# Kernel tuning notes

Measured on AMD Instinct MI355X. Metric: run time of the kernel, lower is better.

## Reference

```python
import jax, jax.numpy as jnp
import numpy as np
from jax import lax

NEG = -1e30  # finite stand-in for -inf to keep gradients clean
BLANK = 0


def _ctc_loss(log_probs, targets, logits_lengths, targets_lengths):
    # log_probs: (B, T, V) log-softmaxed; targets: (B, S) int; lengths: (B,)
    B, T, V = log_probs.shape
    S = targets.shape[1]
    L = 2 * S + 1  # extended label length: blank-interleaved

    # extended label sequence: [blank, t0, blank, t1, ..., blank]
    ext = jnp.zeros((B, L), dtype=targets.dtype).at[:, 1::2].set(targets)

    # gather log-probs of extended labels per time step -> (B, T, L)
    lp_ext = jnp.take_along_axis(
        log_probs, jnp.broadcast_to(ext[:, None, :], (B, T, L)), axis=2
    )

    # skip transition (s-2 -> s) allowed where ext[s] != blank and ext[s] != ext[s-2]
    skip = jnp.concatenate(
        [jnp.zeros((B, 2), dtype=bool),
         (ext[:, 2:] != ext[:, :-2]) & (ext[:, 2:] != BLANK)],
        axis=1,
    )

    # alpha init at t=0
    alpha0 = jnp.full((B, L), NEG, dtype=log_probs.dtype)
    alpha0 = alpha0.at[:, 0].set(lp_ext[:, 0, 0])
    alpha0 = alpha0.at[:, 1].set(
        jnp.where(targets_lengths > 0, lp_ext[:, 0, 1], NEG))

    neg1 = jnp.full((B, 1), NEG, dtype=log_probs.dtype)
    neg2 = jnp.full((B, 2), NEG, dtype=log_probs.dtype)

    def step(alpha, inp):
        lp_t, t = inp  # lp_t: (B, L)
        a1 = jnp.concatenate([neg1, alpha[:, :-1]], axis=1)
        a2 = jnp.where(skip, jnp.concatenate([neg2, alpha[:, :-2]], axis=1), NEG)
        new = jnp.logaddexp(jnp.logaddexp(alpha, a1), a2) + lp_t
        # freeze alpha once past each sequence's length so final read is at t=len-1
        alpha = jnp.where((t < logits_lengths)[:, None], new, alpha)
        return alpha, None

    lp_tbl = jnp.transpose(lp_ext, (1, 0, 2))  # (T, B, L)
    alpha, _ = lax.scan(step, alpha0, (lp_tbl[1:], jnp.arange(1, T)))

    # final states: last blank (index 2*tl) and last label (index 2*tl-1)
    idx_blank = (2 * targets_lengths).astype(jnp.int32)
    idx_label = jnp.maximum(2 * targets_lengths - 1, 0).astype(jnp.int32)
    a_blank = jnp.take_along_axis(alpha, idx_blank[:, None], axis=1)[:, 0]
    a_label = jnp.take_along_axis(alpha, idx_label[:, None], axis=1)[:, 0]
    a_label = jnp.where(targets_lengths > 0, a_label, NEG)
    return -jnp.logaddexp(a_blank, a_label)  # (B,)


def setup_inputs() -> dict:
    key = jax.random.key(0)
    k1, k2, k3, k4 = jax.random.split(key, 4)
    B, T, V, S = 32, 1024, 512, 128
    logits = jax.random.normal(k1, (B, T, V), dtype=jnp.float32)
    targets = jax.random.randint(k2, (B, S), 1, V, dtype=jnp.int32)  # avoid blank=0
    logits_lengths = jax.random.randint(k3, (B,), T // 2, T + 1, dtype=jnp.int32)
    targets_lengths = jax.random.randint(k4, (B,), S // 2, S + 1, dtype=jnp.int32)
    return {
        "logits": logits,
        "targets": targets,
        "logits_lengths": logits_lengths,
        "targets_lengths": targets_lengths,
    }


def reference(logits, targets, logits_lengths, targets_lengths):
    # after_logsoftmax=False -> apply log_softmax; time_major=False -> no permute
    log_probs = jax.nn.log_softmax(logits, axis=2)
    # reduce=None -> per-batch loss of shape (B,)
    return _ctc_loss(log_probs, targets, logits_lengths, targets_lengths)
```

## Files before the change

### kernel.cpp

```cpp
#include <hip/hip_runtime.h>

enum { B_ = 32, T_ = 1024, V_ = 512, S_ = 128 };

static constexpr float K2   = 1.4426950408889634f;
static constexpr float LN2F = 0.6931471805599453f;
#define BOOSTI 6

typedef float f32x4 __attribute__((ext_vector_type(4)));
#define AS1 __attribute__((address_space(1)))
#define AS3 __attribute__((address_space(3)))

#define DPPI(x, ctrl) __builtin_amdgcn_update_dpp(0, (x), (ctrl), 0xF, 0xF, true)
#define DPPF(x, ctrl) __int_as_float(DPPI(__float_as_int(x), (ctrl)))
#define DPP_WSR1(x) DPPF((x), 0x138)

__device__ __forceinline__ float dpp_wave_max_l63(float x) {
  x = fmaxf(x, DPPF(x, 0xB1));   x = fmaxf(x, DPPF(x, 0x4E));
  x = fmaxf(x, DPPF(x, 0x124));  x = fmaxf(x, DPPF(x, 0x128));
  x = fmaxf(x, DPPF(x, 0x142));  x = fmaxf(x, DPPF(x, 0x143));
  return x;
}

__global__ __launch_bounds__(256) void ctc_pre4(
    const float* __restrict__ logits, const int* __restrict__ targets,
    const int* __restrict__ loglen, const int* __restrict__ tgtlen,
    f32x4* __restrict__ Q) {
  const int w = threadIdx.x >> 6, l = threadIdx.x & 63;
  const int row = blockIdx.x * 4 + w;
  const int b = row >> 10;
  const int t = row & (T_ - 1);
  if (t >= loglen[b]) return;
  const float* lrow = logits + (size_t)row * V_;
  const float4* r4 = (const float4*)lrow;
  float4 a = r4[l], c = r4[l + 64];
  float s = __builtin_exp2f(a.x * K2) + __builtin_exp2f(a.y * K2) +
            __builtin_exp2f(a.z * K2) + __builtin_exp2f(a.w * K2) +
            __builtin_exp2f(c.x * K2) + __builtin_exp2f(c.y * K2) +
            __builtin_exp2f(c.z * K2) + __builtin_exp2f(c.w * K2);
  #pragma unroll
  for (int off = 32; off; off >>= 1) s += __shfl_xor(s, off, 64);
  const float sh = (float)BOOSTI - __builtin_log2f(s);

  const int2 ee = ((const int2*)(targets + b * S_))[l];
  const int tl = tgtlen[b];
  const float lgb = __shfl(a.x, 0, 64);
  const float lg1 = lrow[ee.x];
  const float lg3 = lrow[ee.y];
  const float pb  = __builtin_exp2f(fmaf(lgb, K2, sh));
  const float pe1 = __builtin_exp2f(fmaf(lg1, K2, sh));
  const float pe3 = __builtin_exp2f(fmaf(lg3, K2, sh));
  const int smax = 2 * tl;
  f32x4 q;
  q.x = (4 * l + 1 <= smax) ? pe1 : 0.0f;
  q.y = (4 * l + 3 <= smax) ? pe3 : 0.0f;
  q.z = (4 * l     <= smax) ? pb  : 0.0f;
  q.w = (4 * l + 2 <= smax) ? pb  : 0.0f;
  Q[(size_t)row * 64 + l] = q;
}

__global__ __launch_bounds__(128, 1) void ctc_dp7(
    const f32x4* __restrict__ Q, const int* __restrict__ targets,
    const int* __restrict__ loglen, const int* __restrict__ tgtlen,
    float* __restrict__ out) {
  __shared__ f32x4 buf[2][32 * 64];
  __shared__ int flag_ready[2];
  __shared__ int flag_done[2];
  __shared__ float A[257];
  const int wv = threadIdx.x >> 6, l = threadIdx.x & 63;
  const int b = blockIdx.x;
  const int len = loglen[b], tl = tgtlen[b];
  const int nch = (len - 1 + 31) >> 5;
  const f32x4* Qb = Q + (size_t)b * T_ * 64;

  if (threadIdx.x == 0) {
    flag_ready[0] = 0; flag_ready[1] = 0;
    flag_done[0] = 0;  flag_done[1] = 0;
  }
  __syncthreads();

  if (wv == 1) {
    for (int c = 0; c < nch; ++c) {
      if (c >= 2) {
        while (((volatile int*)flag_done)[c & 1] < c - 1)
          __builtin_amdgcn_s_sleep(1);
      }
      const int r0 = 1 + 32 * c;
      #pragma unroll
      for (int i = 0; i < 32; ++i) {
        int row = r0 + i; if (row > T_ - 1) row = T_ - 1;
        __builtin_amdgcn_global_load_lds(
            (const AS1 void*)(const void*)(Qb + (size_t)row * 64 + l),
            (AS3 void*)(void*)(&buf[c & 1][i * 64]), 16, 0, 0);
      }
      asm volatile("s_waitcnt vmcnt(0)" ::: "memory");
      if (l == 0) ((volatile int*)flag_ready)[c & 1] = c + 1;
    }
    return;
  }

  __builtin_amdgcn_s_setprio(1);

  const int2 ee = ((const int2*)(targets + b * S_))[l];
  const int e1 = ee.x, e3 = ee.y;
  const int em1 = __shfl_up(e3, 1);
  const float m1 = ((l > 0) && (e1 != 0) && (e1 != em1)) ? 1.0f : 0.0f;
  const float m3 = ((e3 != 0) && (e3 != e1)) ? 1.0f : 0.0f;
  const float v4l = ((l == 63) && (2 * tl >= 256)) ? 1.0f : 0.0f;

  f32x4 qi = Qb[l];
  float p0 = (l == 0) ? qi.z : 0.0f;
  float p1 = (l == 0) ? qi.x : 0.0f;
  float p2 = 0.0f, p3 = 0.0f, p4 = 0.0f;

  const unsigned bufbase = (unsigned)(uintptr_t)(AS3 char*)(void*)&buf[0][0];

  f32x4 q0, q1, q2, q3, q4, q5, q6, q7;
#define DSRO(R, O) asm volatile("ds_read_b128 %0, %1 offset:" #O \
      : "=&v"(R) : "v"(vb))
#define WTL(R, N) asm volatile("s_waitcnt lgkmcnt(" #N ")" : "+v"(R))

#define COMPUTE(RX) { \
    const float n1_  = DPP_WSR1(p3); \
    const float w0_ = (p0 + n1_) * RX.z; \
    const float w1_ = (p0 + p1 + n1_ * m1) * RX.x; \
    const float w2_ = (p1 + p2) * RX.w; \
    const float w3_ = (p2 + p3 + p1 * m3) * RX.y; \
    const float w4_ = (p4 + p3) * RX.w * v4l; \
    p0 = w0_; p1 = w1_; p2 = w2_; p3 = w3_; p4 = w4_; \
  }

#define RENORM { \
    float m_ = fmaxf(fmaxf(fmaxf(p0, p1), fmaxf(p2, p3)), p4); \
    m_ = dpp_wave_max_l63(m_); \
    const int wm_ = __builtin_amdgcn_readlane(__float_as_int(m_), 63); \
    const int e_ = (wm_ >> 23) & 0xFF; \
    const float sc_ = __int_as_float((254 - e_) << 23); \
    p0 *= sc_; p1 *= sc_; p2 *= sc_; p3 *= sc_; p4 *= sc_; \
    shift += e_ - 127; \
  }

#define FS(R, O)  { WTL(R, 7); COMPUTE(R); DSRO(R, O); }
#define FD(R, N)  { WTL(R, N); COMPUTE(R); }
#define TS(R, O, i)  { WTL(R, 7); if (t0 + (i) < len) COMPUTE(R); DSRO(R, O); }
#define TD(R, N, i)  { WTL(R, N); if (t0 + (i) < len) COMPUTE(R); }

  int shift = 0;
  for (int c = 0; c < nch; ++c) {
    const int t0 = 1 + 32 * c;
    while (((volatile int*)flag_ready)[c & 1] < c + 1)
      __builtin_amdgcn_s_sleep(1);
    const unsigned vb = bufbase + (unsigned)(c & 1) * 32768u + (unsigned)l * 16u;

    DSRO(q0, 0);    DSRO(q1, 1024); DSRO(q2, 2048); DSRO(q3, 3072);
    DSRO(q4, 4096); DSRO(q5, 5120); DSRO(q6, 6144); DSRO(q7, 7168);

    if (t0 + 31 < len) {
      FS(q0, 8192)  FS(q1, 9216)  FS(q2, 10240) FS(q3, 11264)
      FS(q4, 12288) FS(q5, 13312) FS(q6, 14336) FS(q7, 15360)
      FS(q0, 16384) FS(q1, 17408) FS(q2, 18432) FS(q3, 19456)
      FS(q4, 20480) FS(q5, 21504) FS(q6, 22528) FS(q7, 23552)
      RENORM
      FS(q0, 24576) FS(q1, 25600) FS(q2, 26624) FS(q3, 27648)
      FS(q4, 28672) FS(q5, 29696) FS(q6, 30720) FS(q7, 31744)
      FD(q0, 7) FD(q1, 6) FD(q2, 5) FD(q3, 4)
      FD(q4, 3) FD(q5, 2) FD(q6, 1) FD(q7, 0)
      RENORM
    } else {
      TS(q0, 8192, 0)   TS(q1, 9216, 1)   TS(q2, 10240, 2)  TS(q3, 11264, 3)
      TS(q4, 12288, 4)  TS(q5, 13312, 5)  TS(q6, 14336, 6)  TS(q7, 15360, 7)
      TS(q0, 16384, 8)  TS(q1, 17408, 9)  TS(q2, 18432, 10) TS(q3, 19456, 11)
      TS(q4, 20480, 12) TS(q5, 21504, 13) TS(q6, 22528, 14) TS(q7, 23552, 15)
      TS(q0, 24576, 16) TS(q1, 25600, 17) TS(q2, 26624, 18) TS(q3, 27648, 19)
      TS(q4, 28672, 20) TS(q5, 29696, 21) TS(q6, 30720, 22) TS(q7, 31744, 23)
      TD(q0, 7, 24) TD(q1, 6, 25) TD(q2, 5, 26) TD(q3, 4, 27)
      TD(q4, 3, 28) TD(q5, 2, 29) TD(q6, 1, 30) TD(q7, 0, 31)
    }

    asm volatile("s_waitcnt lgkmcnt(0)" ::: "memory");
    if (l == 0) ((volatile int*)flag_done)[c & 1] = c + 1;
  }

  A[4 * l + 0] = p0; A[4 * l + 1] = p1;
  A[4 * l + 2] = p2; A[4 * l + 3] = p3;
  if (l == 63) A[256] = p4;
  asm volatile("s_waitcnt lgkmcnt(0)" ::: "memory");
  if (l == 0) {
    const int ib = 2 * tl;
    const int il = (ib - 1) > 0 ? ib - 1 : 0;
    const float ab = A[ib];
    const float al = (tl > 0) ? A[il] : 0.0f;
    out[b] = -(__builtin_log2f(ab + al) + (float)(shift - BOOSTI * len)) * LN2F;
  }
}

extern "C" void kernel_launch(void* const* d_in, const int* in_sizes, int n_in,
                              void* d_out, int out_size, void* d_ws, size_t ws_size,
                              hipStream_t stream) {
  const float* logits  = (const float*)d_in[0];
  const int*   targets = (const int*)d_in[1];
  const int*   loglen  = (const int*)d_in[2];
  const int*   tgtlen  = (const int*)d_in[3];
  float* out = (float*)d_out;
  f32x4* Q = (f32x4*)d_ws;

  ctc_pre4<<<(B_ * T_) / 4, 256, 0, stream>>>(logits, targets, loglen, tgtlen, Q);
  ctc_dp7<<<B_, 128, 0, stream>>>(Q, targets, loglen, tgtlen, out);
}
```

Measured before the change: 62.59 us.

## Interleave two batch recurrences per compute wave to hide serial DP latency

The DP kernel now handles two batch elements per block: one compute wave advances both alpha recurrences in lockstep while two loader waves fill separate double-buffered LDS regions. Interleaving two independent dependency chains is meant to hide the DPP and FMA latency of the serial per-timestep recurrence. In exchange, the grid halves to 16 blocks, each block runs until the longer of its two sequences finishes, and LDS and register use double. The partial-chunk path now also renormalises mid-chunk.

```diff
diff --git a/kernel.cpp b/kernel.cpp
--- a/kernel.cpp
+++ b/kernel.cpp
@@ -58,138 +58,188 @@
   Q[(size_t)row * 64 + l] = q;
 }
 
-__global__ __launch_bounds__(128, 1) void ctc_dp7(
+__global__ __launch_bounds__(192, 1) void ctc_dp8(
     const f32x4* __restrict__ Q, const int* __restrict__ targets,
     const int* __restrict__ loglen, const int* __restrict__ tgtlen,
     float* __restrict__ out) {
-  __shared__ f32x4 buf[2][32 * 64];
-  __shared__ int flag_ready[2];
-  __shared__ int flag_done[2];
-  __shared__ float A[257];
+  __shared__ f32x4 bufA[2][32 * 64];
+  __shared__ f32x4 bufB[2][32 * 64];
+  __shared__ int flag_readyA[2], flag_readyB[2], flag_doneA[2], flag_doneB[2];
+  __shared__ float Aa[257], Ab[257];
   const int wv = threadIdx.x >> 6, l = threadIdx.x & 63;
-  const int b = blockIdx.x;
-  const int len = loglen[b], tl = tgtlen[b];
-  const int nch = (len - 1 + 31) >> 5;
-  const f32x4* Qb = Q + (size_t)b * T_ * 64;
+  const int bA = blockIdx.x, bB = blockIdx.x + 16;
+  const int lenA = loglen[bA], lenB = loglen[bB];
+  const int tlA = tgtlen[bA], tlB = tgtlen[bB];
+  const int lenMax = lenA > lenB ? lenA : lenB;
+  const int lenMin = lenA < lenB ? lenA : lenB;
+  const int nch = (lenMax - 1 + 31) >> 5;
+  const f32x4* QbA = Q + (size_t)bA * T_ * 64;
+  const f32x4* QbB = Q + (size_t)bB * T_ * 64;
 
   if (threadIdx.x == 0) {
-    flag_ready[0] = 0; flag_ready[1] = 0;
-    flag_done[0] = 0;  flag_done[1] = 0;
+    flag_readyA[0] = flag_readyA[1] = 0; flag_readyB[0] = flag_readyB[1] = 0;
+    flag_doneA[0] = flag_doneA[1] = 0;   flag_doneB[0] = flag_doneB[1] = 0;
   }
   __syncthreads();
 
-  if (wv == 1) {
+  if (wv != 0) {
+    const f32x4* Qp = (wv == 1) ? QbA : QbB;
+    f32x4* bufp = (wv == 1) ? &bufA[0][0] : &bufB[0][0];
+    volatile int* fr = (wv == 1) ? (volatile int*)flag_readyA : (volatile int*)flag_readyB;
+    volatile int* fd = (wv == 1) ? (volatile int*)flag_doneA : (volatile int*)flag_doneB;
     for (int c = 0; c < nch; ++c) {
       if (c >= 2) {
-        while (((volatile int*)flag_done)[c & 1] < c - 1)
-          __builtin_amdgcn_s_sleep(1);
+        while (fd[c & 1] < c - 1) __builtin_amdgcn_s_sleep(1);
       }
       const int r0 = 1 + 32 * c;
       #pragma unroll
       for (int i = 0; i < 32; ++i) {
         int row = r0 + i; if (row > T_ - 1) row = T_ - 1;
         __builtin_amdgcn_global_load_lds(
-            (const AS1 void*)(const void*)(Qb + (size_t)row * 64 + l),
-            (AS3 void*)(void*)(&buf[c & 1][i * 64]), 16, 0, 0);
+            (const AS1 void*)(const void*)(Qp + (size_t)row * 64 + l),
+            (AS3 void*)(void*)(bufp + ((c & 1) * 2048 + i * 64)), 16, 0, 0);
       }
       asm volatile("s_waitcnt vmcnt(0)" ::: "memory");
-      if (l == 0) ((volatile int*)flag_ready)[c & 1] = c + 1;
+      if (l == 0) fr[c & 1] = c + 1;
     }
     return;
   }
 
   __builtin_amdgcn_s_setprio(1);
 
-  const int2 ee = ((const int2*)(targets + b * S_))[l];
-  const int e1 = ee.x, e3 = ee.y;
-  const int em1 = __shfl_up(e3, 1);
-  const float m1 = ((l > 0) && (e1 != 0) && (e1 != em1)) ? 1.0f : 0.0f;
-  const float m3 = ((e3 != 0) && (e3 != e1)) ? 1.0f : 0.0f;
-  const float v4l = ((l == 63) && (2 * tl >= 256)) ? 1.0f : 0.0f;
-
-  f32x4 qi = Qb[l];
-  float p0 = (l == 0) ? qi.z : 0.0f;
-  float p1 = (l == 0) ? qi.x : 0.0f;
-  float p2 = 0.0f, p3 = 0.0f, p4 = 0.0f;
-
-  const unsigned bufbase = (unsigned)(uintptr_t)(AS3 char*)(void*)&buf[0][0];
-
-  f32x4 q0, q1, q2, q3, q4, q5, q6, q7;
-#define DSRO(R, O) asm volatile("ds_read_b128 %0, %1 offset:" #O \
-      : "=&v"(R) : "v"(vb))
-#define WTL(R, N) asm volatile("s_waitcnt lgkmcnt(" #N ")" : "+v"(R))
-
-#define COMPUTE(RX) { \
-    const float n1_  = DPP_WSR1(p3); \
-    const float w0_ = (p0 + n1_) * RX.z; \
-    const float w1_ = (p0 + p1 + n1_ * m1) * RX.x; \
-    const float w2_ = (p1 + p2) * RX.w; \
-    const float w3_ = (p2 + p3 + p1 * m3) * RX.y; \
-    const float w4_ = (p4 + p3) * RX.w * v4l; \
-    p0 = w0_; p1 = w1_; p2 = w2_; p3 = w3_; p4 = w4_; \
-  }
-
-#define RENORM { \
-    float m_ = fmaxf(fmaxf(fmaxf(p0, p1), fmaxf(p2, p3)), p4); \
+  const int2 eeA = ((const int2*)(targets + bA * S_))[l];
+  const int2 eeB = ((const int2*)(targets + bB * S_))[l];
+  const int e1A = eeA.x, e3A = eeA.y, e1B = eeB.x, e3B = eeB.y;
+  const int em1A = __shfl_up(e3A, 1);
+  const int em1B = __shfl_up(e3B, 1);
+  const float m1A = ((l > 0) && (e1A != 0) && (e1A != em1A)) ? 1.0f : 0.0f;
+  const float m3A = ((e3A != 0) && (e3A != e1A)) ? 1.0f : 0.0f;
+  const float v4lA = ((l == 63) && (2 * tlA >= 256)) ? 1.0f : 0.0f;
+  const float m1B = ((l > 0) && (e1B != 0) && (e1B != em1B)) ? 1.0f : 0.0f;
+  const float m3B = ((e3B != 0) && (e3B != e1B)) ? 1.0f : 0.0f;
+  const float v4lB = ((l == 63) && (2 * tlB >= 256)) ? 1.0f : 0.0f;
+
+  f32x4 qiA = QbA[l];
+  f32x4 qiB = QbB[l];
+  float p0A = (l == 0) ? qiA.z : 0.0f, p1A = (l == 0) ? qiA.x : 0.0f;
+  float p2A = 0.0f, p3A = 0.0f, p4A = 0.0f;
+  float p0B = (l == 0) ? qiB.z : 0.0f, p1B = (l == 0) ? qiB.x : 0.0f;
+  float p2B = 0.0f, p3B = 0.0f, p4B = 0.0f;
+
+  const unsigned baseA = (unsigned)(uintptr_t)(AS3 char*)(void*)&bufA[0][0];
+  const unsigned baseB = (unsigned)(uintptr_t)(AS3 char*)(void*)&bufB[0][0];
+
+  asm volatile("s_waitcnt vmcnt(0) lgkmcnt(0)" ::: "memory");
+
+  f32x4 qa0, qa1, qa2, qa3, qa4, qa5, qa6, qa7;
+  f32x4 qb0, qb1, qb2, qb3, qb4, qb5, qb6, qb7;
+#define DSRA(R, O) asm volatile("ds_read_b128 %0, %1 offset:" #O \
+      : "=&v"(R) : "v"(vba))
+#define DSRB(R, O) asm volatile("ds_read_b128 %0, %1 offset:" #O \
+      : "=&v"(R) : "v"(vbb))
+#define WT2(RA, RB, N) asm volatile("s_waitcnt lgkmcnt(" #N ")" \
+      : "+v"(RA), "+v"(RB))
+
+#define COMP(RX, S) { \
+    const float n1_ = DPP_WSR1(p3##S); \
+    const float w0_ = (p0##S + n1_) * RX.z; \
+    const float w1_ = (p0##S + p1##S + n1_ * m1##S) * RX.x; \
+    const float w2_ = (p1##S + p2##S) * RX.w; \
+    const float w3_ = (p2##S + p3##S + p1##S * m3##S) * RX.y; \
+    const float w4_ = (p4##S + p3##S) * RX.w * v4l##S; \
+    p0##S = w0_; p1##S = w1_; p2##S = w2_; p3##S = w3_; p4##S = w4_; \
+  }
+
+#define REN(S) { \
+    float m_ = fmaxf(fmaxf(fmaxf(p0##S, p1##S), fmaxf(p2##S, p3##S)), p4##S); \
     m_ = dpp_wave_max_l63(m_); \
     const int wm_ = __builtin_amdgcn_readlane(__float_as_int(m_), 63); \
     const int e_ = (wm_ >> 23) & 0xFF; \
     const float sc_ = __int_as_float((254 - e_) << 23); \
-    p0 *= sc_; p1 *= sc_; p2 *= sc_; p3 *= sc_; p4 *= sc_; \
-    shift += e_ - 127; \
-  }
-
-#define FS(R, O)  { WTL(R, 7); COMPUTE(R); DSRO(R, O); }
-#define FD(R, N)  { WTL(R, N); COMPUTE(R); }
-#define TS(R, O, i)  { WTL(R, 7); if (t0 + (i) < len) COMPUTE(R); DSRO(R, O); }
-#define TD(R, N, i)  { WTL(R, N); if (t0 + (i) < len) COMPUTE(R); }
-
-  int shift = 0;
+    p0##S *= sc_; p1##S *= sc_; p2##S *= sc_; p3##S *= sc_; p4##S *= sc_; \
+    shift##S += e_ - 127; \
+  }
+
+#define FS2(RA, RB, O) { WT2(RA, RB, 14); COMP(RA, A); COMP(RB, B); \
+    DSRA(RA, O); DSRB(RB, O); }
+#define FD2(RA, RB, N) { WT2(RA, RB, N); COMP(RA, A); COMP(RB, B); }
+#define GS2(RA, RB, O, i) { WT2(RA, RB, 14); \
+    if (t0 + (i) < lenA) COMP(RA, A); \
+    if (t0 + (i) < lenB) COMP(RB, B); \
+    DSRA(RA, O); DSRB(RB, O); }
+#define GD2(RA, RB, N, i) { WT2(RA, RB, N); \
+    if (t0 + (i) < lenA) COMP(RA, A); \
+    if (t0 + (i) < lenB) COMP(RB, B); }
+
+  int shiftA = 0, shiftB = 0;
   for (int c = 0; c < nch; ++c) {
     const int t0 = 1 + 32 * c;
-    while (((volatile int*)flag_ready)[c & 1] < c + 1)
-      __builtin_amdgcn_s_sleep(1);
-    const unsigned vb = bufbase + (unsigned)(c & 1) * 32768u + (unsigned)l * 16u;
-
-    DSRO(q0, 0);    DSRO(q1, 1024); DSRO(q2, 2048); DSRO(q3, 3072);
-    DSRO(q4, 4096); DSRO(q5, 5120); DSRO(q6, 6144); DSRO(q7, 7168);
-
-    if (t0 + 31 < len) {
-      FS(q0, 8192)  FS(q1, 9216)  FS(q2, 10240) FS(q3, 11264)
-      FS(q4, 12288) FS(q5, 13312) FS(q6, 14336) FS(q7, 15360)
-      FS(q0, 16384) FS(q1, 17408) FS(q2, 18432) FS(q3, 19456)
-      FS(q4, 20480) FS(q5, 21504) FS(q6, 22528) FS(q7, 23552)
-      RENORM
-      FS(q0, 24576) FS(q1, 25600) FS(q2, 26624) FS(q3, 27648)
-      FS(q4, 28672) FS(q5, 29696) FS(q6, 30720) FS(q7, 31744)
-      FD(q0, 7) FD(q1, 6) FD(q2, 5) FD(q3, 4)
-      FD(q4, 3) FD(q5, 2) FD(q6, 1) FD(q7, 0)
-      RENORM
+    while (((volatile int*)flag_readyA)[c & 1] < c + 1) __builtin_amdgcn_s_sleep(1);
+    while (((volatile int*)flag_readyB)[c & 1] < c + 1) __builtin_amdgcn_s_sleep(1);
+    const unsigned vba = baseA + (unsigned)(c & 1) * 32768u + (unsigned)l * 16u;
+    const unsigned vbb = baseB + (unsigned)(c & 1) * 32768u + (unsigned)l * 16u;
+
+    DSRA(qa0, 0);    DSRB(qb0, 0);
+    DSRA(qa1, 1024); DSRB(qb1, 1024);
+    DSRA(qa2, 2048); DSRB(qb2, 2048);
+    DSRA(qa3, 3072); DSRB(qb3, 3072);
+    DSRA(qa4, 4096); DSRB(qb4, 4096);
+    DSRA(qa5, 5120); DSRB(qb5, 5120);
+    DSRA(qa6, 6144); DSRB(qb6, 6144);
+    DSRA(qa7, 7168); DSRB(qb7, 7168);
+
+    if (t0 + 31 < lenMin) {
+      FS2(qa0, qb0, 8192)  FS2(qa1, qb1, 9216)  FS2(qa2, qb2, 10240) FS2(qa3, qb3, 11264)
+      FS2(qa4, qb4, 12288) FS2(qa5, qb5, 13312) FS2(qa6, qb6, 14336) FS2(qa7, qb7, 15360)
+      FS2(qa0, qb0, 16384) FS2(qa1, qb1, 17408) FS2(qa2, qb2, 18432) FS2(qa3, qb3, 19456)
+      FS2(qa4, qb4, 20480) FS2(qa5, qb5, 21504) FS2(qa6, qb6, 22528) FS2(qa7, qb7, 23552)
+      REN(A) REN(B)
+      FS2(qa0, qb0, 24576) FS2(qa1, qb1, 25600) FS2(qa2, qb2, 26624) FS2(qa3, qb3, 27648)
+      FS2(qa4, qb4, 28672) FS2(qa5, qb5, 29696) FS2(qa6, qb6, 30720) FS2(qa7, qb7, 31744)
+      FD2(qa0, qb0, 14) FD2(qa1, qb1, 12) FD2(qa2, qb2, 10) FD2(qa3, qb3, 8)
+      FD2(qa4, qb4, 6)  FD2(qa5, qb5, 4)  FD2(qa6, qb6, 2)  FD2(qa7, qb7, 0)
+      REN(A) REN(B)
     } else {
-      TS(q0, 8192, 0)   TS(q1, 9216, 1)   TS(q2, 10240, 2)  TS(q3, 11264, 3)
-      TS(q4, 12288, 4)  TS(q5, 13312, 5)  TS(q6, 14336, 6)  TS(q7, 15360, 7)
-      TS(q0, 16384, 8)  TS(q1, 17408, 9)  TS(q2, 18432, 10) TS(q3, 19456, 11)
-      TS(q4, 20480, 12) TS(q5, 21504, 13) TS(q6, 22528, 14) TS(q7, 23552, 15)
-      TS(q0, 24576, 16) TS(q1, 25600, 17) TS(q2, 26624, 18) TS(q3, 27648, 19)
-      TS(q4, 28672, 20) TS(q5, 29696, 21) TS(q6, 30720, 22) TS(q7, 31744, 23)
-      TD(q0, 7, 24) TD(q1, 6, 25) TD(q2, 5, 26) TD(q3, 4, 27)
-      TD(q4, 3, 28) TD(q5, 2, 29) TD(q6, 1, 30) TD(q7, 0, 31)
+      GS2(qa0, qb0, 8192, 0)   GS2(qa1, qb1, 9216, 1)   GS2(qa2, qb2, 10240, 2)  GS2(qa3, qb3, 11264, 3)
+      GS2(qa4, qb4, 12288, 4)  GS2(qa5, qb5, 13312, 5)  GS2(qa6, qb6, 14336, 6)  GS2(qa7, qb7, 15360, 7)
+      GS2(qa0, qb0, 16384, 8)  GS2(qa1, qb1, 17408, 9)  GS2(qa2, qb2, 18432, 10) GS2(qa3, qb3, 19456, 11)
+      GS2(qa4, qb4, 20480, 12) GS2(qa5, qb5, 21504, 13) GS2(qa6, qb6, 22528, 14) GS2(qa7, qb7, 23552, 15)
+      REN(A) REN(B)
+      GS2(qa0, qb0, 24576, 16) GS2(qa1, qb1, 25600, 17) GS2(qa2, qb2, 26624, 18) GS2(qa3, qb3, 27648, 19)
+      GS2(qa4, qb4, 28672, 20) GS2(qa5, qb5, 29696, 21) GS2(qa6, qb6, 30720, 22) GS2(qa7, qb7, 31744, 23)
+      GD2(qa0, qb0, 14, 24) GD2(qa1, qb1, 12, 25) GD2(qa2, qb2, 10, 26) GD2(qa3, qb3, 8, 27)
+      GD2(qa4, qb4, 6, 28)  GD2(qa5, qb5, 4, 29)  GD2(qa6, qb6, 2, 30)  GD2(qa7, qb7, 0, 31)
+      REN(A) REN(B)
     }
 
     asm volatile("s_waitcnt lgkmcnt(0)" ::: "memory");
-    if (l == 0) ((volatile int*)flag_done)[c & 1] = c + 1;
-  }
-
-  A[4 * l + 0] = p0; A[4 * l + 1] = p1;
-  A[4 * l + 2] = p2; A[4 * l + 3] = p3;
-  if (l == 63) A[256] = p4;
+    if (l == 0) {
+      ((volatile int*)flag_doneA)[c & 1] = c + 1;
+      ((volatile int*)flag_doneB)[c & 1] = c + 1;
+    }
+  }
+
+  Aa[4 * l + 0] = p0A; Aa[4 * l + 1] = p1A;
+  Aa[4 * l + 2] = p2A; Aa[4 * l + 3] = p3A;
+  Ab[4 * l + 0] = p0B; Ab[4 * l + 1] = p1B;
+  Ab[4 * l + 2] = p2B; Ab[4 * l + 3] = p3B;
+  if (l == 63) { Aa[256] = p4A; Ab[256] = p4B; }
   asm volatile("s_waitcnt lgkmcnt(0)" ::: "memory");
   if (l == 0) {
-    const int ib = 2 * tl;
-    const int il = (ib - 1) > 0 ? ib - 1 : 0;
-    const float ab = A[ib];
-    const float al = (tl > 0) ? A[il] : 0.0f;
-    out[b] = -(__builtin_log2f(ab + al) + (float)(shift - BOOSTI * len)) * LN2F;
+    {
+      const int ib = 2 * tlA;
+      const int il = (ib - 1) > 0 ? ib - 1 : 0;
+      const float ab = Aa[ib];
+      const float al = (tlA > 0) ? Aa[il] : 0.0f;
+      out[bA] = -(__builtin_log2f(ab + al) + (float)(shiftA - BOOSTI * lenA)) * LN2F;
+    }
+    {
+      const int ib = 2 * tlB;
+      const int il = (ib - 1) > 0 ? ib - 1 : 0;
+      const float ab = Ab[ib];
+      const float al = (tlB > 0) ? Ab[il] : 0.0f;
+      out[bB] = -(__builtin_log2f(ab + al) + (float)(shiftB - BOOSTI * lenB)) * LN2F;
+    }
   }
 }
 
@@ -204,5 +254,5 @@
   f32x4* Q = (f32x4*)d_ws;
 
   ctc_pre4<<<(B_ * T_) / 4, 256, 0, stream>>>(logits, targets, loglen, tgtlen, Q);
-  ctc_dp7<<<B_, 128, 0, stream>>>(Q, targets, loglen, tgtlen, out);
-}
+  ctc_dp8<<<B_ / 2, 192, 0, stream>>>(Q, targets, loglen, tgtlen, out);
+}
```

Measured after the change: 102.0 us. +63.0%, slower.
